# Optimization experiments

Measured on AMD Instinct MI355X. Metric: run time of the kernel, lower is better.

The kernel has to match this reference:

```python
import jax, jax.numpy as jnp
import numpy as np

B, C, H, W = 4, 64, 256, 256
KH = KW = 3
K = KH * KW
HO, WO = H - 2, W - 2  # VALID 3x3 conv output


def conv2d_valid(x, w, b):
    y = jax.lax.conv_general_dilated(x, w, (1, 1), 'VALID',
                                     dimension_numbers=('NCHW', 'OIHW', 'NCHW'))
    return y + b[None, :, None, None]


def bilinear_gather(x, py, px):
    # x: [B,C,H,W]; py, px: [B,K,HO,WO] fractional sample coords (zero outside).
    y0 = jnp.floor(py)
    x0 = jnp.floor(px)
    ly = py - y0
    lx = px - x0
    y0i = y0.astype(jnp.int32)
    x0i = x0.astype(jnp.int32)
    xf = x.reshape(B, C, H * W)

    def g(yi, xi):
        valid = (yi >= 0) & (yi < H) & (xi >= 0) & (xi < W)
        idx = jnp.clip(yi, 0, H - 1) * W + jnp.clip(xi, 0, W - 1)
        idxf = idx.reshape(B, -1)
        out = jax.vmap(lambda xb, ib: xb[:, ib])(xf, idxf)  # [B,C,K*HO*WO]
        out = out.reshape(B, C, K, HO, WO)
        return out * valid[:, None].astype(x.dtype)

    v = (((1 - ly) * (1 - lx))[:, None] * g(y0i, x0i)
         + ((1 - ly) * lx)[:, None] * g(y0i, x0i + 1)
         + (ly * (1 - lx))[:, None] * g(y0i + 1, x0i)
         + (ly * lx)[:, None] * g(y0i + 1, x0i + 1))
    return v  # [B,C,K,HO,WO]


def deform_conv(x, offset, w, b):
    # offset: [B, 2*K, HO, WO] with channel pairs (dy_k, dx_k), k row-major over 3x3.
    off = offset.reshape(B, K, 2, HO, WO)
    dy, dx = off[:, :, 0], off[:, :, 1]
    kh = (jnp.arange(K) // KW).astype(jnp.float32)
    kw = (jnp.arange(K) % KW).astype(jnp.float32)
    py = jnp.arange(HO, dtype=jnp.float32)[None, None, :, None] + kh[None, :, None, None] + dy
    px = jnp.arange(WO, dtype=jnp.float32)[None, None, None, :] + kw[None, :, None, None] + dx
    s = bilinear_gather(x, py, px)  # [B,C,K,HO,WO]
    out = jnp.einsum('bckhw,ock->bohw', s, w.reshape(w.shape[0], C, K))
    return out + b[None, :, None, None]


def setup_inputs() -> dict:
    key = jax.random.key(0)
    k1, k2, k3 = jax.random.split(key, 3)
    fan = C * KH * KW
    x = jax.random.normal(k1, (B, C, H, W), jnp.float32)
    offset_w = jax.random.normal(k2, (2 * K, C, KH, KW), jnp.float32) * 0.01
    offset_b = jnp.zeros((2 * K,), jnp.float32)
    deform_w = jax.random.normal(k3, (1, C, KH, KW), jnp.float32) * (1.0 / np.sqrt(fan))
    deform_b = jnp.zeros((1,), jnp.float32)
    return {'x': x, 'offset_w': offset_w, 'offset_b': offset_b,
            'deform_w': deform_w, 'deform_b': deform_b}


def reference(x, offset_w, offset_b, deform_w, deform_b):
    offset = conv2d_valid(x, offset_w, offset_b)  # [B,18,HO,WO]
    return deform_conv(x, offset, deform_w, deform_b)  # [B,1,HO,WO]
```

## Files before the change

### kernel.cpp

```cpp
#include <hip/hip_runtime.h>
#include <hip/hip_bf16.h>

#define BB 4
#define CC 64
#define HH 256
#define WW 256
#define KK 9
#define NOFF 18
#define HO 254
#define WO 254
#define NPIX (HO*WO)

typedef __attribute__((ext_vector_type(8))) short bf16x8;
typedef __attribute__((ext_vector_type(4))) float f32x4;

__device__ __align__(16) unsigned char  g_wpack[23552];
__device__ __align__(16) unsigned short g_xT[(size_t)BB * 2 * HH * WW * 32];

#define GLB(p)  ((const __attribute__((address_space(1))) void*)(p))
#define LDSP(p) ((__attribute__((address_space(3))) void*)(p))

static __device__ __forceinline__ unsigned short f2bf(float v) {
    __hip_bfloat16 h = __float2bfloat16(v);
    union { __hip_bfloat16 b; unsigned short u; } cv; cv.b = h; return cv.u;
}
static __device__ __forceinline__ float bf2f(unsigned short u) {
    unsigned int w = ((unsigned int)u) << 16;
    float f; __builtin_memcpy(&f, &w, 4); return f;
}

static __device__ __forceinline__ void repack_piece(
    int tap, int tid, int nthr,
    const float* __restrict__ offset_w,
    const float* __restrict__ deform_w)
{
    if (tap < 9) {
        for (int i = tid; i < 18 * 64; i += nthr) {
            int o = i >> 6;
            int c = i & 63;
            int row = tap * 18 + o;
            unsigned int byte = (unsigned)(row * 128 + c * 2) ^ (((unsigned)(row & 7)) << 4);
            *(unsigned short*)(g_wpack + byte) = f2bf(offset_w[((size_t)o * CC + c) * KK + tap]);
        }
    } else {
        for (int i = tid; i < 16 * 64; i += nthr) {
            int t = i >> 6;
            int c = i & 63;
            float v = (t < KK) ? deform_w[(size_t)c * KK + t] : 0.0f;
            unsigned int byte = (unsigned)(t * 128 + c * 2) ^ (((unsigned)(t & 7)) << 4);
            *(unsigned short*)(g_wpack + 20736 + byte) = f2bf(v);
        }
    }
}

__global__ __launch_bounds__(256) void transpose_kernel(
    const float* __restrict__ x,
    const float* __restrict__ offset_w,
    const float* __restrict__ deform_w)
{
    __shared__ float s[64][65];
    const int tid = threadIdx.x;
    const int w0 = blockIdx.x * 64;
    const int h  = blockIdx.y;
    const int b  = blockIdx.z;

    if (b == 0 && blockIdx.x == 0 && h < 10)
        repack_piece(h, tid, 256, offset_w, deform_w);

    #pragma unroll
    for (int it = 0; it < 4; ++it) {
        int i  = tid + it * 256;
        int c  = i >> 4;
        int p4 = (i & 15) << 2;
        float4 v = *(const float4*)(x + (((size_t)b * CC + c) * HH + h) * WW + w0 + p4);
        s[c][p4 + 0] = v.x; s[c][p4 + 1] = v.y; s[c][p4 + 2] = v.z; s[c][p4 + 3] = v.w;
    }
    __syncthreads();
    #pragma unroll
    for (int it = 0; it < 2; ++it) {
        int j  = tid + it * 256;
        int px = j >> 3;
        int g  = j & 7;
        unsigned int u[4];
        #pragma unroll
        for (int q = 0; q < 4; ++q) {
            __hip_bfloat162 h2 = __float22bfloat162_rn(
                make_float2(s[g * 8 + 2 * q][px], s[g * 8 + 2 * q + 1][px]));
            __builtin_memcpy(&u[q], &h2, 4);
        }
        const int half = g >> 2;
        unsigned short* dst = g_xT
            + ((size_t)(b * 2 + half) * HH * WW + (size_t)h * WW + w0 + px) * 32 + (g & 3) * 8;
        *(uint4*)dst = make_uint4(u[0], u[1], u[2], u[3]);
    }
}

#define PTF 20
#define NCF 400
#define ROWB 1280
#define PATCHB (20*ROWB)
#define LDS_P0 0
#define LDS_P1 PATCHB
#define SMEM_F (2*PATCHB)
#define LDS_SOFF 0
#define LDS_SY   18504

__global__ __launch_bounds__(256) void conv_gather_fused(
    const float* __restrict__ offset_b,
    const float* __restrict__ deform_w,
    const float* __restrict__ deform_b,
    float* __restrict__ out)
{
    __shared__ __align__(16) unsigned char smem[SMEM_F];
    const int tid = threadIdx.x;
    const int wv = tid >> 6;
    const int l  = tid & 63;
    const int lr = l & 15;
    const int lk = l >> 4;

    const int x0 = blockIdx.x * 16;
    const int y0 = blockIdx.y * 16;
    const int b  = blockIdx.z;

    auto stage_half = [&](int h, int ldsbase) {
        const unsigned char* hb = (const unsigned char*)(g_xT + (size_t)(b * 2 + h) * HH * WW * 32);
        for (int k = wv; k < 25; k += 4) {
            unsigned p = (unsigned)(k * 1024 + (l << 4));
            unsigned s = p ^ (((p >> 7) & 7u) << 4);
            int r    = (int)(s / (unsigned)ROWB);
            int pl   = (int)(s % (unsigned)ROWB);
            int cell = pl >> 6;
            int within = pl & 63;
            int gy = min(max(y0 - 1 + r, 0), HH - 1);
            int gx = min(max(x0 - 1 + cell, 0), WW - 1);
            __builtin_amdgcn_global_load_lds(GLB(hb + ((size_t)gy * WW + gx) * 64 + within),
                                             LDSP(smem + ldsbase + k * 1024), 16, 0, 0);
        }
    };
    stage_half(0, LDS_P0);
    stage_half(1, LDS_P1);
    __syncthreads();

    const int o1 = (16 + lr > 17) ? 17 : 16 + lr;
    const float bias0 = offset_b[lr];
    const float bias1 = (lr < 2) ? offset_b[16 + lr] : 0.0f;

    f32x4 accC[4][2];
    f32x4 accY[7];
    #pragma unroll
    for (int mi = 0; mi < 4; ++mi)
        #pragma unroll
        for (int reg = 0; reg < 4; ++reg) { accC[mi][0][reg] = bias0; accC[mi][1][reg] = bias1; }
    #pragma unroll
    for (int j = 0; j < 7; ++j) accY[j] = (f32x4){0.f, 0.f, 0.f, 0.f};

    auto ldw = [&](int row, int cbyte) -> bf16x8 {
        unsigned int byte = (unsigned)(row * 128 + cbyte) ^ (((unsigned)(row & 7)) << 4);
        return *(const bf16x8*)(g_wpack + byte);
    };
    auto lda = [&](int ldsbase, int cell) -> bf16x8 {
        unsigned lin = (unsigned)(cell * 64 + lk * 16);
        lin ^= ((lin >> 7) & 7u) << 4;
        return *(const bf16x8*)(smem + ldsbase + lin);
    };

    #pragma unroll
    for (int h = 0; h < 2; ++h) {
        const int pbase_lds = h ? LDS_P1 : LDS_P0;
        const int cbyte = h * 64 + lk * 16;
        #pragma unroll
        for (int kw = 0; kw < 3; ++kw) {
            #pragma unroll
            for (int kh = 0; kh < 3; ++kh) {
                const int tap = kh * 3 + kw;
                bf16x8 b0 = ldw(tap * 18 + lr, cbyte);
                bf16x8 b1 = ldw(tap * 18 + o1, cbyte);
                #pragma unroll
                for (int mi = 0; mi < 4; ++mi) {
                    const int cell = (4 * wv + mi + kh + 1) * PTF + (lr + kw + 1);
                    bf16x8 a = lda(pbase_lds, cell);
                    accC[mi][0] = __builtin_amdgcn_mfma_f32_16x16x32_bf16(a, b0, accC[mi][0], 0, 0, 0);
                    accC[mi][1] = __builtin_amdgcn_mfma_f32_16x16x32_bf16(a, b1, accC[mi][1], 0, 0, 0);
                }
            }
        }
        {
            unsigned int byY = (unsigned)(lr * 128 + cbyte) ^ (((unsigned)(lr & 7)) << 4);
            bf16x8 bY = *(const bf16x8*)(g_wpack + 20736 + byY);
            #pragma unroll
            for (int j = 0; j < 7; ++j) {
                const int t = wv + 4 * j;
                if (t < 25) {
                    bf16x8 a = lda(pbase_lds, t * 16 + lr);
                    accY[j] = __builtin_amdgcn_mfma_f32_16x16x32_bf16(a, bY, accY[j], 0, 0, 0);
                }
            }
        }
    }

    __syncthreads();

    float* s_off = (float*)(smem + LDS_SOFF);
    float* s_Y   = (float*)(smem + LDS_SY);
    #pragma unroll
    for (int mi = 0; mi < 4; ++mi) {
        #pragma unroll
        for (int nt = 0; nt < 2; ++nt) {
            const int o = nt * 16 + lr;
            if (o < NOFF) {
                const int pbase = (4 * wv + mi) * 16 + lk * 4;
                #pragma unroll
                for (int reg = 0; reg < 4; ++reg)
                    s_off[o * 257 + pbase + reg] = accC[mi][nt][reg];
            }
        }
    }
    #pragma unroll
    for (int j = 0; j < 7; ++j) {
        const int t = wv + 4 * j;
        if (t < 25 && lr < KK) {
            #pragma unroll
            for (int reg = 0; reg < 4; ++reg) {
                const int cell = t * 16 + lk * 4 + reg;
                int r = cell / PTF, col = cell - r * PTF;
                int gy = y0 - 1 + r, gx = x0 - 1 + col;
                bool inimg = (gy >= 0 && gy < HH && gx >= 0 && gx < WW);
                s_Y[lr * 401 + cell] = inimg ? accY[j][reg] : 0.0f;
            }
        }
    }
    __syncthreads();

    const int ty = tid >> 4, tx = tid & 15;
    const int ho = y0 + ty, wo = x0 + tx;
    if (ho >= HO || wo >= WO) return;

    float acc = deform_b[0];

    #pragma unroll
    for (int k = 0; k < KK; ++k) {
        const int kh = k / 3, kw = k % 3;
        float dy = s_off[(2 * k) * 257 + tid];
        float dx = s_off[(2 * k + 1) * 257 + tid];
        float py = (float)(ho + kh) + dy;
        float px = (float)(wo + kw) + dx;
        float y0f = floorf(py), x0f = floorf(px);
        float ly = py - y0f, lx = px - x0f;
        int yi0 = (int)y0f, xi0 = (int)x0f;
        int ry = yi0 - (y0 - 1);
        int rx = xi0 - (x0 - 1);
        float w00 = (1.0f - ly) * (1.0f - lx);
        float w01 = (1.0f - ly) * lx;
        float w10 = ly * (1.0f - lx);
        float w11 = ly * lx;
        float g;
        if ((unsigned)ry <= (unsigned)(PTF - 2) && (unsigned)rx <= (unsigned)(PTF - 2)) {
            const float* tp = s_Y + k * 401;
            const int id = ry * PTF + rx;
            g = w00 * tp[id]       + w01 * tp[id + 1]
              + w10 * tp[id + PTF] + w11 * tp[id + PTF + 1];
        } else {
            int yi1 = yi0 + 1, xi1 = xi0 + 1;
            float m00 = (yi0 >= 0 && yi0 < HH && xi0 >= 0 && xi0 < WW) ? w00 : 0.0f;
            float m01 = (yi0 >= 0 && yi0 < HH && xi1 >= 0 && xi1 < WW) ? w01 : 0.0f;
            float m10 = (yi1 >= 0 && yi1 < HH && xi0 >= 0 && xi0 < WW) ? w10 : 0.0f;
            float m11 = (yi1 >= 0 && yi1 < HH && xi1 >= 0 && xi1 < WW) ? w11 : 0.0f;
            int y0c = min(max(yi0, 0), HH - 1), y1c = min(max(yi1, 0), HH - 1);
            int x0c = min(max(xi0, 0), WW - 1), x1c = min(max(xi1, 0), WW - 1);
            g = 0.0f;
            #pragma unroll
            for (int h = 0; h < 2; ++h) {
                const unsigned short* xh = g_xT + (size_t)(b * 2 + h) * HH * WW * 32;
                const unsigned short* p00 = xh + (size_t)(y0c * WW + x0c) * 32;
                const unsigned short* p01 = xh + (size_t)(y0c * WW + x1c) * 32;
                const unsigned short* p10 = xh + (size_t)(y1c * WW + x0c) * 32;
                const unsigned short* p11 = xh + (size_t)(y1c * WW + x1c) * 32;
                for (int c = 0; c < 32; ++c) {
                    float gc = m00 * bf2f(p00[c]) + m01 * bf2f(p01[c])
                             + m10 * bf2f(p10[c]) + m11 * bf2f(p11[c]);
                    g = fmaf(gc, deform_w[(size_t)(h * 32 + c) * KK + k], g);
                }
            }
        }
        acc += g;
    }

    out[(size_t)b * NPIX + ho * WO + wo] = acc;
}

extern "C" void kernel_launch(void* const* d_in, const int* in_sizes, int n_in,
                              void* d_out, int out_size, void* d_ws, size_t ws_size,
                              hipStream_t stream) {
    const float* x        = (const float*)d_in[0];
    const float* offset_w = (const float*)d_in[1];
    const float* offset_b = (const float*)d_in[2];
    const float* deform_w = (const float*)d_in[3];
    const float* deform_b = (const float*)d_in[4];
    float* out = (float*)d_out;

    hipLaunchKernelGGL(transpose_kernel, dim3(4, 256, BB), dim3(256), 0, stream,
                       x, offset_w, deform_w);
    hipLaunchKernelGGL(conv_gather_fused, dim3(16, 16, BB), dim3(256), 0, stream,
                       offset_b, deform_w, deform_b, out);
}
```

Baseline: 43.84 us.

## Single-buffer LDS patch staging to cut shared memory and raise occupancy

The fused conv/gather kernel now stages the two channel halves one after the other into a single LDS patch buffer instead of two. Each half is loaded and consumed by MFMAs before the next is loaded. LDS drops from about 51 KB to about 33 KB per block, which may allow more resident blocks per CU. The cost is that the two loads no longer overlap and extra barriers serialize the second half's load behind the first half's compute.

```diff
diff --git a/kernel.cpp b/kernel.cpp
--- a/kernel.cpp
+++ b/kernel.cpp
@@ -99,11 +99,9 @@
 #define NCF 400
 #define ROWB 1280
 #define PATCHB (20*ROWB)
-#define LDS_P0 0
-#define LDS_P1 PATCHB
-#define SMEM_F (2*PATCHB)
 #define LDS_SOFF 0
 #define LDS_SY   18504
+#define SMEM_F   32944
 
 __global__ __launch_bounds__(256) void conv_gather_fused(
     const float* __restrict__ offset_b,
@@ -122,7 +120,7 @@
     const int y0 = blockIdx.y * 16;
     const int b  = blockIdx.z;
 
-    auto stage_half = [&](int h, int ldsbase) {
+    auto stage_half = [&](int h) {
         const unsigned char* hb = (const unsigned char*)(g_xT + (size_t)(b * 2 + h) * HH * WW * 32);
         for (int k = wv; k < 25; k += 4) {
             unsigned p = (unsigned)(k * 1024 + (l << 4));
@@ -134,12 +132,9 @@
             int gy = min(max(y0 - 1 + r, 0), HH - 1);
             int gx = min(max(x0 - 1 + cell, 0), WW - 1);
             __builtin_amdgcn_global_load_lds(GLB(hb + ((size_t)gy * WW + gx) * 64 + within),
-                                             LDSP(smem + ldsbase + k * 1024), 16, 0, 0);
+                                             LDSP(smem + k * 1024), 16, 0, 0);
         }
     };
-    stage_half(0, LDS_P0);
-    stage_half(1, LDS_P1);
-    __syncthreads();
 
     const int o1 = (16 + lr > 17) ? 17 : 16 + lr;
     const float bias0 = offset_b[lr];
@@ -158,15 +153,13 @@
         unsigned int byte = (unsigned)(row * 128 + cbyte) ^ (((unsigned)(row & 7)) << 4);
         return *(const bf16x8*)(g_wpack + byte);
     };
-    auto lda = [&](int ldsbase, int cell) -> bf16x8 {
+    auto lda = [&](int cell) -> bf16x8 {
         unsigned lin = (unsigned)(cell * 64 + lk * 16);
         lin ^= ((lin >> 7) & 7u) << 4;
-        return *(const bf16x8*)(smem + ldsbase + lin);
+        return *(const bf16x8*)(smem + lin);
     };
 
-    #pragma unroll
-    for (int h = 0; h < 2; ++h) {
-        const int pbase_lds = h ? LDS_P1 : LDS_P0;
+    auto mfma_half = [&](int h) {
         const int cbyte = h * 64 + lk * 16;
         #pragma unroll
         for (int kw = 0; kw < 3; ++kw) {
@@ -178,7 +171,7 @@
                 #pragma unroll
                 for (int mi = 0; mi < 4; ++mi) {
                     const int cell = (4 * wv + mi + kh + 1) * PTF + (lr + kw + 1);
-                    bf16x8 a = lda(pbase_lds, cell);
+                    bf16x8 a = lda(cell);
                     accC[mi][0] = __builtin_amdgcn_mfma_f32_16x16x32_bf16(a, b0, accC[mi][0], 0, 0, 0);
                     accC[mi][1] = __builtin_amdgcn_mfma_f32_16x16x32_bf16(a, b1, accC[mi][1], 0, 0, 0);
                 }
@@ -191,13 +184,20 @@
             for (int j = 0; j < 7; ++j) {
                 const int t = wv + 4 * j;
                 if (t < 25) {
-                    bf16x8 a = lda(pbase_lds, t * 16 + lr);
+                    bf16x8 a = lda(t * 16 + lr);
                     accY[j] = __builtin_amdgcn_mfma_f32_16x16x32_bf16(a, bY, accY[j], 0, 0, 0);
                 }
             }
         }
-    }
-
+    };
+
+    stage_half(0);
+    __syncthreads();
+    mfma_half(0);
+    __syncthreads();
+    stage_half(1);
+    __syncthreads();
+    mfma_half(1);
     __syncthreads();
 
     float* s_off = (float*)(smem + LDS_SOFF);
```

After: 45.17 us. 1.03x slower.
